# Kernel tuning notes

Measured on AMD Instinct MI355X. Metric: run time of the kernel, lower is better.

Reference implementation:

```python
import jax, jax.numpy as jnp
import numpy as np
import math

N_HEADS = 16
ROPE_BASE = 10000.0


def _apply_rope(x_bshd, cosA, sinA):
    # x_bshd: [B,S,H,dh]; cosA/sinA: [S, dh//2]
    x1 = x_bshd[..., ::2]
    x2 = x_bshd[..., 1::2]
    c = cosA[None, :, None, :]
    s = sinA[None, :, None, :]
    # interleave rotated pairs back: [..., dh//2, 2] -> [..., dh]
    out = jnp.stack([x1 * c - x2 * s, x1 * s + x2 * c], axis=-1)
    return out.reshape(x_bshd.shape)


def setup_inputs() -> dict:
    key = jax.random.key(0)
    k1, k2, k3 = jax.random.split(key, 3)
    B, S, D = 4, 2048, 2048
    std = 1.0 / math.sqrt(D)
    x = jax.random.normal(k1, (B, S, D), dtype=jnp.float32)
    qkv_w = jax.random.normal(k2, (3 * D, D), dtype=jnp.float32) * std
    qkv_b = jnp.zeros((3 * D,), dtype=jnp.float32)
    out_w = jax.random.normal(k3, (D, D), dtype=jnp.float32) * std
    out_b = jnp.zeros((D,), dtype=jnp.float32)
    return {"x": x, "qkv_w": qkv_w, "qkv_b": qkv_b, "out_w": out_w, "out_b": out_b}


def reference(x, qkv_w, qkv_b, out_w, out_b):
    B, S, D = x.shape
    H = N_HEADS
    dh = D // H
    # fused QKV projection
    qkv = x @ qkv_w.T + qkv_b                      # [B,S,3D]
    q, k, v = jnp.split(qkv, 3, axis=-1)
    q = q.reshape(B, S, H, dh)
    k = k.reshape(B, S, H, dh)
    v = v.reshape(B, S, H, dh)
    # RoPE (interleaved pairs, base 10000)
    freqs = 1.0 / (ROPE_BASE ** (jnp.arange(0, dh, 2, dtype=jnp.float32) / dh))
    angles = jnp.arange(S, dtype=jnp.float32)[:, None] * freqs[None, :]  # [S, dh//2]
    cosA, sinA = jnp.cos(angles), jnp.sin(angles)
    q = _apply_rope(q, cosA, sinA)
    k = _apply_rope(k, cosA, sinA)
    # causal SDPA
    scale = 1.0 / math.sqrt(dh)
    scores = jnp.einsum('bshd,bthd->bhst', q, k) * scale  # [B,H,S,S]
    causal = jnp.tril(jnp.ones((S, S), dtype=bool))
    scores = jnp.where(causal[None, None], scores, jnp.finfo(scores.dtype).min)
    attn = jax.nn.softmax(scores, axis=-1)
    y = jnp.einsum('bhst,bthd->bshd', attn, v).reshape(B, S, D)
    return y @ out_w.T + out_b
```

## Files before the change

### kernel.cpp

```cpp
#include <hip/hip_runtime.h>
#include <hip/hip_bf16.h>
#include <math.h>

typedef __bf16 bf16x8 __attribute__((ext_vector_type(8)));
typedef float f32x4 __attribute__((ext_vector_type(4)));

#define GPTR(x) ((const __attribute__((address_space(1))) void*)(x))
#define LPTR(x) ((__attribute__((address_space(3))) void*)(x))

__device__ __forceinline__ void gload_lds16(const void* g, void* l) {
  __builtin_amdgcn_global_load_lds(GPTR(g), LPTR(l), 16, 0, 0);
}

__global__ __launch_bounds__(256) void cast_f32_bf16(const float* __restrict__ in,
                                                     __hip_bfloat16* __restrict__ out,
                                                     int n4) {
  int i = blockIdx.x * 256 + threadIdx.x;
  if (i >= n4) return;
  float4 v = ((const float4*)in)[i];
  __hip_bfloat16 t[4];
  t[0] = __float2bfloat16(v.x); t[1] = __float2bfloat16(v.y);
  t[2] = __float2bfloat16(v.z); t[3] = __float2bfloat16(v.w);
  ((uint2*)out)[i] = *(uint2*)t;
}

__global__ __launch_bounds__(256) void rope_tables(float* __restrict__ cosT,
                                                   float* __restrict__ sinT, int S) {
  int i = blockIdx.x * 256 + threadIdx.x;
  if (i >= S * 64) return;
  int j = i & 63, s = i >> 6;
  float freq = powf(10000.0f, -(float)(2 * j) * (1.0f / 128.0f));
  float a = (float)s * freq;
  cosT[i] = cosf(a);
  sinT[i] = sinf(a);
}

__global__ __launch_bounds__(256) void rope_apply(__hip_bfloat16* __restrict__ qkv,
                                                  const float* __restrict__ cosT,
                                                  const float* __restrict__ sinT) {
  int i = blockIdx.x * 256 + threadIdx.x;
  int jc = i & 15;
  int h = (i >> 4) & 15;
  int row = i >> 8;
  int s = row & 2047;
  float4 c4 = *(const float4*)&cosT[s * 64 + jc * 4];
  float4 s4 = *(const float4*)&sinT[s * 64 + jc * 4];
  size_t base = (size_t)row * 6144 + h * 128 + jc * 8;
#pragma unroll
  for (int half = 0; half < 2; half++) {
    __hip_bfloat16* p = qkv + base + half * 2048;
    bf16x8 v = *(bf16x8*)p;
    bf16x8 o;
    float cc[4] = {c4.x, c4.y, c4.z, c4.w};
    float ss[4] = {s4.x, s4.y, s4.z, s4.w};
#pragma unroll
    for (int u = 0; u < 4; u++) {
      float x1 = (float)v[2 * u], x2 = (float)v[2 * u + 1];
      o[2 * u]     = (__bf16)(x1 * cc[u] - x2 * ss[u]);
      o[2 * u + 1] = (__bf16)(x1 * ss[u] + x2 * cc[u]);
    }
    *(bf16x8*)p = o;
  }
}

template <int OUT_BF16>
__global__ __launch_bounds__(256) void gemm_bt(const __hip_bfloat16* __restrict__ A,
                                               const __hip_bfloat16* __restrict__ Bm,
                                               const float* __restrict__ bias,
                                               void* __restrict__ Cv,
                                               int M, int N, int K) {
  __shared__ __align__(16) __hip_bfloat16 Asm[128 * 32];
  __shared__ __align__(16) __hip_bfloat16 Bsm[128 * 32];
  const int tid = threadIdx.x, wave = tid >> 6, lane = tid & 63;
  const int bm = blockIdx.y * 128, bn = blockIdx.x * 128;
  const int wm = (wave >> 1) * 64, wn = (wave & 1) * 64;
  f32x4 acc[4][4] = {};
  const int fr = lane & 15, fk = (lane >> 4) * 8;

  const int srow = wave * 32 + (lane >> 2);
  const size_t rowbytes = (size_t)K * 2;
  const char* Ag = (const char*)(A + (size_t)(bm + srow) * K) + (lane & 3) * 16;
  const char* Bg = (const char*)(Bm + (size_t)(bn + srow) * K) + (lane & 3) * 16;
  __hip_bfloat16* As0 = &Asm[(wave * 32) * 32];
  __hip_bfloat16* Bs0 = &Bsm[(wave * 32) * 32];

  for (int k0 = 0; k0 < K; k0 += 32) {
    const size_t kb = (size_t)k0 * 2;
    gload_lds16(Ag + kb, As0);
    gload_lds16(Ag + kb + 16 * rowbytes, &As0[16 * 32]);
    gload_lds16(Bg + kb, Bs0);
    gload_lds16(Bg + kb + 16 * rowbytes, &Bs0[16 * 32]);
    __syncthreads();
    bf16x8 af[4], bfr[4];
#pragma unroll
    for (int t = 0; t < 4; t++) af[t] = *(const bf16x8*)&Asm[(wm + t * 16 + fr) * 32 + fk];
#pragma unroll
    for (int t = 0; t < 4; t++) bfr[t] = *(const bf16x8*)&Bsm[(wn + t * 16 + fr) * 32 + fk];
#pragma unroll
    for (int i = 0; i < 4; i++)
#pragma unroll
      for (int j = 0; j < 4; j++)
        acc[i][j] = __builtin_amdgcn_mfma_f32_16x16x32_bf16(af[i], bfr[j], acc[i][j], 0, 0, 0);
    __syncthreads();
  }

  const int r0 = bm + wm + (lane >> 4) * 4;
  const int c0 = bn + wn + (lane & 15);
#pragma unroll
  for (int i = 0; i < 4; i++) {
#pragma unroll
    for (int j = 0; j < 4; j++) {
      const int col = c0 + j * 16;
      const float bv = bias[col];
#pragma unroll
      for (int r = 0; r < 4; r++) {
        const int row = r0 + i * 16 + r;
        float v = acc[i][j][r] + bv;
        if (OUT_BF16)
          ((__hip_bfloat16*)Cv)[(size_t)row * N + col] = __float2bfloat16(v);
        else
          ((float*)Cv)[(size_t)row * N + col] = v;
      }
    }
  }
}

#define VTS 72
__global__ __launch_bounds__(512, 4) void flash_attn(const __hip_bfloat16* __restrict__ qkv,
                                                     __hip_bfloat16* __restrict__ y,
                                                     int S) {
  __shared__ __align__(16) char Ksm[64 * 256];
  __shared__ __align__(16) __hip_bfloat16 Vts[128 * VTS];
  const int tid = threadIdx.x, wave = tid >> 6, lane = tid & 63;
  const int l15 = lane & 15, g = lane >> 4;
  const int b = blockIdx.y >> 4, h = blockIdx.y & 15;
  const int pi = blockIdx.x;
  const size_t ldq = 6144;
  const __hip_bfloat16* Qb = qkv + (size_t)b * S * ldq + (size_t)h * 128;
  const __hip_bfloat16* Kb = Qb + 2048;
  const __hip_bfloat16* Vb = Qb + 4096;

  const int posj = ((lane >> 5) << 5) | ((((lane >> 2) & 3)) << 3) |
                   (((lane >> 4) & 1) << 2) | (lane & 3);

  for (int pass = 0; pass < 2; ++pass) {
    const int qt = pass == 0 ? (15 - pi) : pi;
    const int q0 = qt * 128;
    const int qr = q0 + wave * 16 + l15;
    const int rmin = q0 + wave * 16, rmax = rmin + 15;

    bf16x8 aq[4];
    {
      const __hip_bfloat16* qp = Qb + (size_t)qr * ldq + g * 8;
#pragma unroll
      for (int c = 0; c < 4; c++) aq[c] = *(const bf16x8*)(qp + c * 32);
    }

    float m_r = -1e30f, l_r = 0.f;
    f32x4 oacc[8] = {};
    const int nT = q0 / 64 + 2;

    int4 kreg[2], vreg[2];
#pragma unroll
    for (int i = 0; i < 2; i++) {
      int chunk = tid + i * 512, krow = chunk >> 4, kc16 = chunk & 15;
      kreg[i] = *(const int4*)((const char*)(Kb + (size_t)krow * ldq) + kc16 * 16);
      int dc = wave + 8 * i;
      vreg[i] = *(const int4*)(Vb + (size_t)lane * ldq + dc * 8);
    }

    for (int t = 0; t < nT; ++t) {
      const int kv0 = t * 64;
      __syncthreads();
#pragma unroll
      for (int i = 0; i < 2; i++) {
        int chunk = tid + i * 512, krow = chunk >> 4, kc16 = chunk & 15;
        *(int4*)&Ksm[krow * 256 + ((kc16 ^ (krow & 7)) * 16)] = kreg[i];
        int dc = wave + 8 * i;
        const __hip_bfloat16* e = (const __hip_bfloat16*)&vreg[i];
#pragma unroll
        for (int u = 0; u < 8; u++) Vts[(dc * 8 + u) * VTS + posj] = e[u];
      }
      __syncthreads();
      if (t + 1 < nT) {
        const int nkv = kv0 + 64;
#pragma unroll
        for (int i = 0; i < 2; i++) {
          int chunk = tid + i * 512, krow = chunk >> 4, kc16 = chunk & 15;
          kreg[i] = *(const int4*)((const char*)(Kb + (size_t)(nkv + krow) * ldq) + kc16 * 16);
          int dc = wave + 8 * i;
          vreg[i] = *(const int4*)(Vb + (size_t)(nkv + lane) * ldq + dc * 8);
        }
      }
      if (kv0 > rmax) continue;

      f32x4 sacc[4];
      __builtin_amdgcn_s_setprio(1);
#pragma unroll
      for (int nf = 0; nf < 4; nf++) {
        f32x4 a = {0.f, 0.f, 0.f, 0.f};
        const int n = nf * 16 + l15;
#pragma unroll
        for (int c = 0; c < 4; c++) {
          int cc = c * 4 + g;
          bf16x8 kf = *(const bf16x8*)&Ksm[n * 256 + ((cc ^ (n & 7)) * 16)];
          a = __builtin_amdgcn_mfma_f32_16x16x32_bf16(kf, aq[c], a, 0, 0, 0);
        }
        sacc[nf] = a;
      }
      __builtin_amdgcn_s_setprio(0);

      if (kv0 + 63 > rmin) {
#pragma unroll
        for (int nf = 0; nf < 4; nf++)
#pragma unroll
          for (int r = 0; r < 4; r++)
            if (kv0 + nf * 16 + g * 4 + r > qr) sacc[nf][r] = -3e38f;
      }

      const float t2e = 0.12751744f;
      float mx = sacc[0][0];
#pragma unroll
      for (int nf = 0; nf < 4; nf++)
#pragma unroll
        for (int r = 0; r < 4; r++) mx = fmaxf(mx, sacc[nf][r]);
      mx = fmaxf(mx, __shfl_xor(mx, 16, 64));
      mx = fmaxf(mx, __shfl_xor(mx, 32, 64));
      float mnew = fmaxf(m_r, mx);
      float corr = __builtin_amdgcn_exp2f((m_r - mnew) * t2e);
      m_r = mnew;
      float sum = 0.f;
#pragma unroll
      for (int nf = 0; nf < 4; nf++)
#pragma unroll
        for (int r = 0; r < 4; r++) {
          float pv = __builtin_amdgcn_exp2f((sacc[nf][r] - m_r) * t2e);
          sacc[nf][r] = pv;
          sum += pv;
        }
      sum += __shfl_xor(sum, 16, 64);
      sum += __shfl_xor(sum, 32, 64);
      l_r = l_r * corr + sum;
#pragma unroll
      for (int of = 0; of < 8; of++)
#pragma unroll
        for (int r = 0; r < 4; r++) oacc[of][r] *= corr;

      bf16x8 pa0, pa1;
#pragma unroll
      for (int r = 0; r < 4; r++) {
        pa0[r]     = (__bf16)sacc[0][r];
        pa0[r + 4] = (__bf16)sacc[1][r];
        pa1[r]     = (__bf16)sacc[2][r];
        pa1[r + 4] = (__bf16)sacc[3][r];
      }

      __builtin_amdgcn_s_setprio(1);
#pragma unroll
      for (int of = 0; of < 8; of++) {
        const int vrow = of * 16 + l15;
        bf16x8 v0 = *(const bf16x8*)&Vts[vrow * VTS + g * 8];
        bf16x8 v1 = *(const bf16x8*)&Vts[vrow * VTS + 32 + g * 8];
        oacc[of] = __builtin_amdgcn_mfma_f32_16x16x32_bf16(v0, pa0, oacc[of], 0, 0, 0);
        oacc[of] = __builtin_amdgcn_mfma_f32_16x16x32_bf16(v1, pa1, oacc[of], 0, 0, 0);
      }
      __builtin_amdgcn_s_setprio(0);
    }

    const float inv = 1.0f / l_r;
    __hip_bfloat16* yp = y + ((size_t)b * S + qr) * 2048 + h * 128;
#pragma unroll
    for (int of = 0; of < 8; of++) {
      __hip_bfloat16 o4[4];
#pragma unroll
      for (int r = 0; r < 4; r++) o4[r] = __float2bfloat16(oacc[of][r] * inv);
      *(uint2*)&yp[of * 16 + g * 4] = *(uint2*)o4;
    }
  }
}

extern "C" void kernel_launch(void* const* d_in, const int* in_sizes, int n_in,
                              void* d_out, int out_size, void* d_ws, size_t ws_size,
                              hipStream_t stream) {
  const float* x = (const float*)d_in[0];
  const float* qkv_w = (const float*)d_in[1];
  const float* qkv_b = (const float*)d_in[2];
  const float* out_w = (const float*)d_in[3];
  const float* out_b = (const float*)d_in[4];
  float* out = (float*)d_out;

  const int B = 4, S = 2048, D = 2048;
  const int M = B * S;

  char* ws = (char*)d_ws;
  __hip_bfloat16* xb   = (__hip_bfloat16*)(ws + 0);
  __hip_bfloat16* wqb  = (__hip_bfloat16*)(ws + 33554432);
  __hip_bfloat16* wob  = (__hip_bfloat16*)(ws + 58720256);
  __hip_bfloat16* qkvb = (__hip_bfloat16*)(ws + 67108864);
  __hip_bfloat16* yb   = (__hip_bfloat16*)(ws + 167772160);
  float* cosT          = (float*)(ws + 201326592);
  float* sinT          = (float*)(ws + 201850880);

  cast_f32_bf16<<<M * D / 4 / 256, 256, 0, stream>>>(x, xb, M * D / 4);
  cast_f32_bf16<<<3 * D * D / 4 / 256, 256, 0, stream>>>(qkv_w, wqb, 3 * D * D / 4);
  cast_f32_bf16<<<D * D / 4 / 256, 256, 0, stream>>>(out_w, wob, D * D / 4);
  rope_tables<<<S * 64 / 256, 256, 0, stream>>>(cosT, sinT, S);

  dim3 g1(3 * D / 128, M / 128);
  gemm_bt<1><<<g1, 256, 0, stream>>>(xb, wqb, qkv_b, (void*)qkvb, M, 3 * D, D);

  rope_apply<<<M, 256, 0, stream>>>(qkvb, cosT, sinT);

  dim3 g2(8, B * 16);
  flash_attn<<<g2, 512, 0, stream>>>(qkvb, yb, S);

  dim3 g3(D / 128, M / 128);
  gemm_bt<0><<<g3, 256, 0, stream>>>(yb, wob, out_b, (void*)out, M, D, D);
}
```

Baseline: 724.8 us.

## Rewrite GEMM with 256x256 tiles, double-buffered swizzled LDS and MFMA priority

Replaces the 128x128 single-buffered GEMM with a 256x256-tile, 512-thread kernel that uses a K-step of 64. The kernel double-buffers 128KB of LDS and prefetches the next K-tile in phases interleaved with the MFMA work. LDS addresses use an XOR swizzle to avoid bank conflicts, and s_setprio raises priority around the MFMA blocks. The goal is more data reuse per global load and overlap of loads with compute. The cost is 128KB of LDS per block, which limits occupancy to one block per CU, plus higher register pressure.

Result: faster. 590.7 us (-18.5%).

```diff
diff --git a/kernel.cpp b/kernel.cpp
--- a/kernel.cpp
+++ b/kernel.cpp
@@ -64,58 +64,84 @@
 }
 
 template <int OUT_BF16>
-__global__ __launch_bounds__(256) void gemm_bt(const __hip_bfloat16* __restrict__ A,
-                                               const __hip_bfloat16* __restrict__ Bm,
-                                               const float* __restrict__ bias,
-                                               void* __restrict__ Cv,
-                                               int M, int N, int K) {
-  __shared__ __align__(16) __hip_bfloat16 Asm[128 * 32];
-  __shared__ __align__(16) __hip_bfloat16 Bsm[128 * 32];
-  const int tid = threadIdx.x, wave = tid >> 6, lane = tid & 63;
-  const int bm = blockIdx.y * 128, bn = blockIdx.x * 128;
-  const int wm = (wave >> 1) * 64, wn = (wave & 1) * 64;
-  f32x4 acc[4][4] = {};
-  const int fr = lane & 15, fk = (lane >> 4) * 8;
-
-  const int srow = wave * 32 + (lane >> 2);
-  const size_t rowbytes = (size_t)K * 2;
-  const char* Ag = (const char*)(A + (size_t)(bm + srow) * K) + (lane & 3) * 16;
-  const char* Bg = (const char*)(Bm + (size_t)(bn + srow) * K) + (lane & 3) * 16;
-  __hip_bfloat16* As0 = &Asm[(wave * 32) * 32];
-  __hip_bfloat16* Bs0 = &Bsm[(wave * 32) * 32];
-
-  for (int k0 = 0; k0 < K; k0 += 32) {
-    const size_t kb = (size_t)k0 * 2;
-    gload_lds16(Ag + kb, As0);
-    gload_lds16(Ag + kb + 16 * rowbytes, &As0[16 * 32]);
-    gload_lds16(Bg + kb, Bs0);
-    gload_lds16(Bg + kb + 16 * rowbytes, &Bs0[16 * 32]);
+__global__ __launch_bounds__(512, 2) void gemm256(const __hip_bfloat16* __restrict__ A,
+                                                  const __hip_bfloat16* __restrict__ Bm,
+                                                  const float* __restrict__ bias,
+                                                  void* __restrict__ Cv,
+                                                  int M, int N, int K) {
+  __shared__ __align__(16) char lds[2][65536];
+  const int tid = threadIdx.x, wave = tid >> 6;
+  const int lane = tid & 63, l15 = lane & 15, g = lane >> 4;
+  const int bm = blockIdx.y * 256, bn = blockIdx.x * 256;
+  const int wr = wave >> 2, wc = wave & 3;
+  f32x4 acc[8][4] = {};
+
+  auto stage = [&](int t, int bufx, int matB, int half) {
+#pragma unroll
+    for (int j = 0; j < 2; j++) {
+      const int rl = j * 64 + (tid >> 3);
+      const int c = tid & 7;
+      const int row = half * 128 + rl;
+      const __hip_bfloat16* src =
+          (matB ? Bm + (size_t)(bn + row) * K : A + (size_t)(bm + row) * K)
+          + (size_t)t * 64 + ((c ^ (row & 7)) << 3);
+      char* dst = &lds[bufx][matB * 32768 + half * 16384 + ((j * 512 + (wave << 6)) << 4)];
+      gload_lds16(src, dst);
+    }
+  };
+
+  const int nK = K >> 6;
+  stage(0, 0, 0, 0); stage(0, 0, 0, 1); stage(0, 0, 1, 0); stage(0, 0, 1, 1);
+  __syncthreads();
+
+  int cur = 0;
+  for (int t = 0; t < nK; ++t) {
+    const int nb = cur ^ 1;
+    const bool more = (t + 1 < nK);
+#pragma unroll
+    for (int ph = 0; ph < 4; ph++) {
+      const int mh = ph & 1, kh = ph >> 1;
+      if (ph == 0 && more) { stage(t + 1, nb, 0, 0); stage(t + 1, nb, 0, 1); }
+      if (ph == 1 && more) stage(t + 1, nb, 1, 0);
+      if (ph == 2 && more) stage(t + 1, nb, 1, 1);
+      bf16x8 af[4], bfr[4];
+#pragma unroll
+      for (int i = 0; i < 4; i++) {
+        const int row = wr * 128 + (mh * 4 + i) * 16 + l15;
+        const int c = (kh * 4 + g) ^ (row & 7);
+        af[i] = *(const bf16x8*)&lds[cur][row * 128 + c * 16];
+      }
+#pragma unroll
+      for (int j = 0; j < 4; j++) {
+        const int col = wc * 64 + j * 16 + l15;
+        const int c = (kh * 4 + g) ^ (col & 7);
+        bfr[j] = *(const bf16x8*)&lds[cur][32768 + col * 128 + c * 16];
+      }
+      __builtin_amdgcn_s_setprio(1);
+#pragma unroll
+      for (int i = 0; i < 4; i++)
+#pragma unroll
+        for (int j = 0; j < 4; j++)
+          acc[mh * 4 + i][j] = __builtin_amdgcn_mfma_f32_16x16x32_bf16(
+              af[i], bfr[j], acc[mh * 4 + i][j], 0, 0, 0);
+      __builtin_amdgcn_s_setprio(0);
+    }
     __syncthreads();
-    bf16x8 af[4], bfr[4];
-#pragma unroll
-    for (int t = 0; t < 4; t++) af[t] = *(const bf16x8*)&Asm[(wm + t * 16 + fr) * 32 + fk];
-#pragma unroll
-    for (int t = 0; t < 4; t++) bfr[t] = *(const bf16x8*)&Bsm[(wn + t * 16 + fr) * 32 + fk];
-#pragma unroll
-    for (int i = 0; i < 4; i++)
-#pragma unroll
-      for (int j = 0; j < 4; j++)
-        acc[i][j] = __builtin_amdgcn_mfma_f32_16x16x32_bf16(af[i], bfr[j], acc[i][j], 0, 0, 0);
-    __syncthreads();
+    cur = nb;
   }
 
-  const int r0 = bm + wm + (lane >> 4) * 4;
-  const int c0 = bn + wn + (lane & 15);
-#pragma unroll
-  for (int i = 0; i < 4; i++) {
-#pragma unroll
-    for (int j = 0; j < 4; j++) {
-      const int col = c0 + j * 16;
+  const int r0 = bm + wr * 128 + g * 4;
+  const int c0 = bn + wc * 64 + l15;
+#pragma unroll
+  for (int fi = 0; fi < 8; fi++) {
+#pragma unroll
+    for (int fj = 0; fj < 4; fj++) {
+      const int col = c0 + fj * 16;
       const float bv = bias[col];
 #pragma unroll
       for (int r = 0; r < 4; r++) {
-        const int row = r0 + i * 16 + r;
-        float v = acc[i][j][r] + bv;
+        const int row = r0 + fi * 16 + r;
+        float v = acc[fi][fj][r] + bv;
         if (OUT_BF16)
           ((__hip_bfloat16*)Cv)[(size_t)row * N + col] = __float2bfloat16(v);
         else
@@ -306,14 +332,14 @@
   cast_f32_bf16<<<D * D / 4 / 256, 256, 0, stream>>>(out_w, wob, D * D / 4);
   rope_tables<<<S * 64 / 256, 256, 0, stream>>>(cosT, sinT, S);
 
-  dim3 g1(3 * D / 128, M / 128);
-  gemm_bt<1><<<g1, 256, 0, stream>>>(xb, wqb, qkv_b, (void*)qkvb, M, 3 * D, D);
+  dim3 g1(3 * D / 256, M / 256);
+  gemm256<1><<<g1, 512, 0, stream>>>(xb, wqb, qkv_b, (void*)qkvb, M, 3 * D, D);
 
   rope_apply<<<M, 256, 0, stream>>>(qkvb, cosT, sinT);
 
   dim3 g2(8, B * 16);
   flash_attn<<<g2, 512, 0, stream>>>(qkvb, yb, S);
 
-  dim3 g3(D / 128, M / 128);
-  gemm_bt<0><<<g3, 256, 0, stream>>>(yb, wob, out_b, (void*)out, M, D, D);
-}
+  dim3 g3(D / 256, M / 256);
+  gemm256<0><<<g3, 512, 0, stream>>>(yb, wob, out_b, (void*)out, M, D, D);
+}
```
